# Performance work log

Measured on AMD Instinct MI355X. Metric: run time of the kernel, lower is better.

## Reference

```python
import jax, jax.numpy as jnp
import numpy as np

B, L = 2, 1024
V, D_MODEL, NL = 32, 256, 6
DI, DS, DC, DTR = 512, 16, 4, 16  # d_inner=expand*d_model, d_state, d_conv, dt_rank=d_model/16
NC, MAXL = 10, 2048
ALPHA = 0.1  # observer_alpha


def setup_inputs() -> dict:
    key = jax.random.key(0)
    ks = jax.random.split(key, 16)
    std = 0.02
    emb = std * jax.random.normal(ks[0], (V, D_MODEL), jnp.float32)
    emb = emb.at[0].set(0.0)  # padding_idx=0
    pos_emb = std * jax.random.normal(ks[1], (MAXL, D_MODEL), jnp.float32)
    ln_w = jnp.ones((NL, D_MODEL), jnp.float32)
    ln_b = jnp.zeros((NL, D_MODEL), jnp.float32)
    in_proj_w = std * jax.random.normal(ks[2], (NL, 2 * DI, D_MODEL), jnp.float32)
    conv_w = 0.1 * jax.random.normal(ks[3], (NL, DI, DC), jnp.float32)
    conv_b = jnp.zeros((NL, DI), jnp.float32)
    x_proj_w = std * jax.random.normal(ks[4], (NL, DTR + 2 * DS, DI), jnp.float32)
    dt_proj_w = std * jax.random.normal(ks[5], (NL, DI, DTR), jnp.float32)
    dt_proj_b = jnp.full((NL, DI), -4.6, jnp.float32)  # softplus(-4.6) ~ 0.01 init dt
    A_log = jnp.broadcast_to(jnp.log(jnp.arange(1, DS + 1, dtype=jnp.float32)), (NL, DI, DS)).copy()  # S4D-real
    Dp = jnp.ones((NL, DI), jnp.float32)
    out_proj_w = std * jax.random.normal(ks[6], (NL, D_MODEL, DI), jnp.float32)
    norm_w = jnp.ones((D_MODEL,), jnp.float32)
    norm_b = jnp.zeros((D_MODEL,), jnp.float32)
    cls_w = std * jax.random.normal(ks[7], (NC, D_MODEL), jnp.float32)
    cls_b = jnp.zeros((NC,), jnp.float32)
    x = jax.random.randint(ks[8], (B, L), 0, V, jnp.int64 if jax.config.jax_enable_x64 else jnp.int32)
    mask = jnp.ones((B, L), jnp.int32)
    return dict(emb=emb, pos_emb=pos_emb, ln_w=ln_w, ln_b=ln_b, in_proj_w=in_proj_w,
                conv_w=conv_w, conv_b=conv_b, x_proj_w=x_proj_w, dt_proj_w=dt_proj_w,
                dt_proj_b=dt_proj_b, A_log=A_log, Dp=Dp, out_proj_w=out_proj_w,
                norm_w=norm_w, norm_b=norm_b, cls_w=cls_w, cls_b=cls_b, x=x, mask=mask)


def _ln(x, w, b):
    m = x.mean(-1, keepdims=True)
    v = ((x - m) ** 2).mean(-1, keepdims=True)
    return (x - m) / jnp.sqrt(v + 1e-5) * w + b


def _forward(emb, pos_emb, ln_w, ln_b, in_proj_w, conv_w, conv_b, x_proj_w,
             dt_proj_w, dt_proj_b, A_log, Dp, out_proj_w, norm_w, norm_b,
             cls_w, cls_b, x, mask):
    Bsz, Lsz = x.shape
    h = emb[x] + pos_emb[:Lsz][None, :, :]  # [B,L,D]
    for i in range(NL):
        res = h
        hn = _ln(h, ln_w[i], ln_b[i])
        xz = hn @ in_proj_w[i].T                      # [B,L,2*DI]
        x_in, z = jnp.split(xz, 2, axis=-1)
        # causal depthwise conv1d, kernel DC
        xpad = jnp.pad(x_in, ((0, 0), (DC - 1, 0), (0, 0)))
        xc = conv_b[i]
        for k in range(DC):
            xc = xc + conv_w[i][:, k] * xpad[:, k:k + Lsz, :]
        xc = jax.nn.silu(xc)
        x_dbl = xc @ x_proj_w[i].T                    # [B,L,DTR+2*DS]
        dt = x_dbl[..., :DTR]
        Bm = x_dbl[..., DTR:DTR + DS]
        Cm = x_dbl[..., DTR + DS:]
        delta = jax.nn.softplus(dt @ dt_proj_w[i].T + dt_proj_b[i])  # [B,L,DI]
        A = -jnp.exp(A_log[i])                        # [DI,DS]
        dA = jnp.exp(delta[..., None] * A)            # [B,L,DI,DS]
        dBu = delta[..., None] * Bm[:, :, None, :] * xc[..., None]

        def step(carry, inp):
            hs, hh = carry
            dA_t, dBu_t, c_t = inp
            hs = dA_t * hs + dBu_t                    # true state
            pred = dA_t * hh + dBu_t                  # observer prediction
            hh = pred + ALPHA * (hs - pred)           # Luenberger correction
            y = jnp.einsum('bdn,bn->bd', hh, c_t)
            return (hs, hh), y

        init = (jnp.zeros((Bsz, DI, DS), xc.dtype), jnp.zeros((Bsz, DI, DS), xc.dtype))
        _, ys = jax.lax.scan(step, init,
                             (jnp.moveaxis(dA, 1, 0), jnp.moveaxis(dBu, 1, 0), jnp.moveaxis(Cm, 1, 0)))
        y = jnp.moveaxis(ys, 0, 1) + Dp[i] * xc       # [B,L,DI]
        y = y * jax.nn.silu(z)
        h = y @ out_proj_w[i].T + res
    mf = mask[..., None].astype(h.dtype)
    pooled = (h * mf).sum(axis=1) / mf.sum(axis=1)    # masked mean pool
    pooled = _ln(pooled, norm_w, norm_b)
    return pooled @ cls_w.T + cls_b                   # [B,NC]


def reference(emb, pos_emb, ln_w, ln_b, in_proj_w, conv_w, conv_b, x_proj_w,
              dt_proj_w, dt_proj_b, A_log, Dp, out_proj_w, norm_w, norm_b,
              cls_w, cls_b, x, mask):
    return _forward(emb, pos_emb, ln_w, ln_b, in_proj_w, conv_w, conv_b, x_proj_w,
                    dt_proj_w, dt_proj_b, A_log, Dp, out_proj_w, norm_w, norm_b,
                    cls_w, cls_b, x, mask)
```

## Files before the change

### kernel.cpp

```cpp
#include <hip/hip_runtime.h>
#include <math.h>

#define B_ 2
#define L_ 1024
#define DM 256
#define NL_ 6
#define DI_ 512
#define DS_ 16
#define DC_ 4
#define NC_ 10
#define ALPHA_ 0.1f
#define LC 32
#define NCH (L_/LC)
#define NCHAIN (B_*DI_*DS_)
#define BETA_LC 0.034336838202925124f

typedef unsigned short ushort_t;
typedef __attribute__((ext_vector_type(8))) short s16x8;
typedef __attribute__((ext_vector_type(4))) float f32x4;
typedef __attribute__((ext_vector_type(8))) unsigned short u16x8;

__device__ __forceinline__ float sigmoidf_(float x){ return 1.f/(1.f+__expf(-x)); }
__device__ __forceinline__ ushort_t f2bf(float f){
  union{float f;unsigned u;} c; c.f=f; unsigned u=c.u;
  return (ushort_t)((u + 0x7fffu + ((u>>16)&1u))>>16);
}
__device__ __forceinline__ float bf2f(ushort_t h){
  union{unsigned u;float f;} c; c.u = ((unsigned)h)<<16; return c.f;
}
__device__ __forceinline__ int kidx(int d){ return d + ((d>>7)<<2); }

__global__ void k_embed(const float* __restrict__ emb, const float* __restrict__ pos,
                        const int* __restrict__ ids, float* __restrict__ h){
  int row = blockIdx.x;
  int t = row & (L_-1);
  int d = threadIdx.x;
  int v = ids[row];
  h[(size_t)row*DM + d] = emb[(size_t)v*DM + d] + pos[(size_t)t*DM + d];
}

__global__ void k_cvt2(const float* __restrict__ a, int na, const float* __restrict__ b2,
                       ushort_t* __restrict__ oa, ushort_t* __restrict__ ob, int ntot){
  int i = (blockIdx.x*256 + threadIdx.x)*4;
  if (i >= ntot) return;
  const float* src; ushort_t* dst; int k;
  if (i < na){ src = a; dst = oa; k = i; }
  else       { src = b2; dst = ob; k = i - na; }
  float4 v = *reinterpret_cast<const float4*>(&src[k]);
  ushort4 r;
  r.x = f2bf(v.x); r.y = f2bf(v.y); r.z = f2bf(v.z); r.w = f2bf(v.w);
  *reinterpret_cast<ushort4*>(&dst[k]) = r;
}

__global__ __launch_bounds__(256) void k_gemm_ln(const float* __restrict__ h,
    const ushort_t* __restrict__ W, const float* __restrict__ lw,
    const float* __restrict__ lb, ushort_t* __restrict__ xzb){
  __shared__ ushort_t As[64][264];
  __shared__ ushort_t Ws[64][264];
  int bm = blockIdx.y<<6, bn = blockIdx.x<<6;
  int tid = threadIdx.x;
  {
    int r = tid>>2, q = tid&3;
    const float* src = &h[(size_t)(bm+r)*DM + q*64];
    float4 v[16]; float s1=0.f, s2=0.f;
    #pragma unroll
    for (int i=0;i<16;i++){
      v[i] = *reinterpret_cast<const float4*>(src + i*4);
      s1 += v[i].x+v[i].y+v[i].z+v[i].w;
      s2 += v[i].x*v[i].x+v[i].y*v[i].y+v[i].z*v[i].z+v[i].w*v[i].w;
    }
    s1 += __shfl_xor(s1,1); s2 += __shfl_xor(s2,1);
    s1 += __shfl_xor(s1,2); s2 += __shfl_xor(s2,2);
    float mean = s1*(1.f/DM);
    float rstd = rsqrtf(s2*(1.f/DM) - mean*mean + 1e-5f);
    #pragma unroll
    for (int i=0;i<16;i++){
      int c = q*64 + i*4;
      ushort4 o;
      o.x = f2bf((v[i].x-mean)*rstd*lw[c+0]+lb[c+0]);
      o.y = f2bf((v[i].y-mean)*rstd*lw[c+1]+lb[c+1]);
      o.z = f2bf((v[i].z-mean)*rstd*lw[c+2]+lb[c+2]);
      o.w = f2bf((v[i].w-mean)*rstd*lw[c+3]+lb[c+3]);
      *reinterpret_cast<ushort4*>(&As[r][c]) = o;
    }
    const ushort_t* ws = &W[(size_t)(bn+r)*DM + q*64];
    #pragma unroll
    for (int i=0;i<8;i++)
      *reinterpret_cast<u16x8*>(&Ws[r][q*64+i*8]) = *reinterpret_cast<const u16x8*>(ws + i*8);
  }
  __syncthreads();
  int lane = tid&63, wid = tid>>6;
  int wm = (wid>>1)<<5, wn = (wid&1)<<5;
  int fr = lane&15, fk = (lane>>4)<<3;
  f32x4 acc[2][2] = {};
  #pragma unroll
  for (int k0=0;k0<DM;k0+=32){
    s16x8 a0 = *reinterpret_cast<const s16x8*>(&As[wm+fr][k0+fk]);
    s16x8 a1 = *reinterpret_cast<const s16x8*>(&As[wm+16+fr][k0+fk]);
    s16x8 b0 = *reinterpret_cast<const s16x8*>(&Ws[wn+fr][k0+fk]);
    s16x8 b1 = *reinterpret_cast<const s16x8*>(&Ws[wn+16+fr][k0+fk]);
    acc[0][0] = __builtin_amdgcn_mfma_f32_16x16x32_bf16(a0,b0,acc[0][0],0,0,0);
    acc[0][1] = __builtin_amdgcn_mfma_f32_16x16x32_bf16(a0,b1,acc[0][1],0,0,0);
    acc[1][0] = __builtin_amdgcn_mfma_f32_16x16x32_bf16(a1,b0,acc[1][0],0,0,0);
    acc[1][1] = __builtin_amdgcn_mfma_f32_16x16x32_bf16(a1,b1,acc[1][1],0,0,0);
  }
  int cr = (lane>>4)<<2, cc = lane&15;
  #pragma unroll
  for (int i=0;i<2;i++)
    #pragma unroll
    for (int j=0;j<2;j++){
      int row = bm + wm + (i<<4) + cr;
      int col = bn + wn + (j<<4) + cc;
      #pragma unroll
      for (int r=0;r<4;r++)
        xzb[(size_t)(row+r)*(2*DI_) + col] = f2bf(acc[i][j][r]);
    }
}

__global__ __launch_bounds__(256) void k_xpc(const ushort_t* __restrict__ xzb,
    const float* __restrict__ cw, const float* __restrict__ cb,
    const float* __restrict__ xw, const float* __restrict__ dtw,
    const float* __restrict__ dtb, ushort_t* __restrict__ xcb,
    float* __restrict__ xdbl, ushort_t* __restrict__ deltab){
  __shared__ float sxz[7][DI_];
  __shared__ float sx[4][DI_+16];
  __shared__ float sdbl[4][48];
  int tid = threadIdx.x;
  int m0 = blockIdx.x*4;
  #pragma unroll
  for (int idx=0; idx<14; ++idx){
    int flat = idx*256 + tid;
    int i = flat>>9, d = flat&511;
    int mr = m0 - 3 + i;
    sxz[i][d] = (mr>=0) ? bf2f(xzb[(size_t)mr*(2*DI_) + d]) : 0.f;
  }
  __syncthreads();
  #pragma unroll
  for (int idx=0; idx<8; ++idx){
    int flat = idx*256 + tid;
    int r = flat>>9, d = flat&511;
    int t = (m0 + r) & (L_-1);
    float acc = cb[d];
    #pragma unroll
    for (int k=0;k<4;k++)
      if (t-3+k >= 0) acc = fmaf(cw[d*4+k], sxz[r+k][d], acc);
    float sv = acc * sigmoidf_(acc);
    sx[r][kidx(d)] = sv;
    xcb[(size_t)(m0+r)*DI_ + d] = f2bf(sv);
  }
  __syncthreads();
  if (tid < 192){
    int o = tid>>2, q = tid&3;
    const float* wp = &xw[(size_t)o*DI_ + q*128];
    const int qb = q*132;
    float a0=0.f,a1=0.f,a2=0.f,a3=0.f;
    #pragma unroll 8
    for (int k4=0;k4<32;k4++){
      float4 wv = *reinterpret_cast<const float4*>(wp + k4*4);
      int kk = qb + k4*4;
      float4 x0 = *reinterpret_cast<const float4*>(&sx[0][kk]);
      float4 x1 = *reinterpret_cast<const float4*>(&sx[1][kk]);
      float4 x2 = *reinterpret_cast<const float4*>(&sx[2][kk]);
      float4 x3 = *reinterpret_cast<const float4*>(&sx[3][kk]);
      a0 = fmaf(x0.x,wv.x,a0); a0 = fmaf(x0.y,wv.y,a0); a0 = fmaf(x0.z,wv.z,a0); a0 = fmaf(x0.w,wv.w,a0);
      a1 = fmaf(x1.x,wv.x,a1); a1 = fmaf(x1.y,wv.y,a1); a1 = fmaf(x1.z,wv.z,a1); a1 = fmaf(x1.w,wv.w,a1);
      a2 = fmaf(x2.x,wv.x,a2); a2 = fmaf(x2.y,wv.y,a2); a2 = fmaf(x2.z,wv.z,a2); a2 = fmaf(x2.w,wv.w,a2);
      a3 = fmaf(x3.x,wv.x,a3); a3 = fmaf(x3.y,wv.y,a3); a3 = fmaf(x3.z,wv.z,a3); a3 = fmaf(x3.w,wv.w,a3);
    }
    a0 += __shfl_xor(a0,1); a0 += __shfl_xor(a0,2);
    a1 += __shfl_xor(a1,1); a1 += __shfl_xor(a1,2);
    a2 += __shfl_xor(a2,1); a2 += __shfl_xor(a2,2);
    a3 += __shfl_xor(a3,1); a3 += __shfl_xor(a3,2);
    if (q==0){
      sdbl[0][o]=a0; sdbl[1][o]=a1; sdbl[2][o]=a2; sdbl[3][o]=a3;
      xdbl[(size_t)(m0+0)*48+o]=a0;
      xdbl[(size_t)(m0+1)*48+o]=a1;
      xdbl[(size_t)(m0+2)*48+o]=a2;
      xdbl[(size_t)(m0+3)*48+o]=a3;
    }
  }
  __syncthreads();
  #pragma unroll
  for (int idx=0; idx<8; ++idx){
    int flat = idx*256 + tid;
    int r = flat>>9, n = flat&511;
    const float4* wp = reinterpret_cast<const float4*>(&dtw[n*16]);
    float4 w0=wp[0], w1=wp[1], w2=wp[2], w3=wp[3];
    const float* sd = sdbl[r];
    float acc = dtb[n];
    acc = fmaf(sd[0],w0.x,acc);  acc = fmaf(sd[1],w0.y,acc);
    acc = fmaf(sd[2],w0.z,acc);  acc = fmaf(sd[3],w0.w,acc);
    acc = fmaf(sd[4],w1.x,acc);  acc = fmaf(sd[5],w1.y,acc);
    acc = fmaf(sd[6],w1.z,acc);  acc = fmaf(sd[7],w1.w,acc);
    acc = fmaf(sd[8],w2.x,acc);  acc = fmaf(sd[9],w2.y,acc);
    acc = fmaf(sd[10],w2.z,acc); acc = fmaf(sd[11],w2.w,acc);
    acc = fmaf(sd[12],w3.x,acc); acc = fmaf(sd[13],w3.y,acc);
    acc = fmaf(sd[14],w3.z,acc); acc = fmaf(sd[15],w3.w,acc);
    float sp2 = (acc>20.f)? acc : log1pf(__expf(acc));
    deltab[(size_t)(m0+r)*DI_ + n] = f2bf(sp2);
  }
}

__global__ __launch_bounds__(256) void k_scanA(const ushort_t* __restrict__ deltab,
    const ushort_t* __restrict__ xcb, const float* __restrict__ xdbl,
    const float* __restrict__ A_log, float4* __restrict__ smry){
  int j = blockIdx.x, g = blockIdx.y, b = blockIdx.z;
  int tid = threadIdx.x;
  int n = tid&15, dg = tid>>4;
  int d0 = g*16;
  __shared__ float sdel[LC][16], sxv[LC][16], sB[LC][16];
  if (tid < 128){
    int arr = tid>>6, slot = tid&63, row = slot>>1, half = slot&1;
    int m = b*L_ + j*LC + row;
    const ushort_t* src = arr ? xcb : deltab;
    u16x8 v = *reinterpret_cast<const u16x8*>(&src[(size_t)m*DI_ + d0 + half*8]);
    float* dst = arr ? &sxv[row][half*8] : &sdel[row][half*8];
    #pragma unroll
    for (int i=0;i<8;i++) dst[i] = bf2f((ushort_t)v[i]);
  } else {
    int slot = tid-128;
    int row = slot>>2, c4 = (slot&3)<<2;
    int m = b*L_ + j*LC + row;
    *reinterpret_cast<float4*>(&sB[row][c4]) =
      *reinterpret_cast<const float4*>(&xdbl[(size_t)m*48 + 16 + c4]);
  }
  __syncthreads();
  float a = -__expf(A_log[(d0+dg)*DS_ + n]);
  float hs=0.f, hh=0.f, cp=1.f;
  #pragma unroll
  for (int tt=0; tt<LC; tt+=8){
    float dA8[8], dBu8[8];
    #pragma unroll
    for (int t=0;t<8;t++){
      float dv = sdel[tt+t][dg];
      dA8[t]  = __expf(dv*a);
      dBu8[t] = dv * sxv[tt+t][dg] * sB[tt+t][n];
    }
    #pragma unroll
    for (int t=0;t<8;t++){
      float mix = fmaf(ALPHA_, hs-hh, hh);
      hs = fmaf(dA8[t], hs, dBu8[t]);
      hh = fmaf(dA8[t], mix, dBu8[t]);
      cp *= dA8[t];
    }
  }
  smry[(size_t)j*NCHAIN + (size_t)(b*DI_+d0)*DS_ + tid] = float4{cp,hs,hh,0.f};
}

__global__ __launch_bounds__(256) void k_scanC(const ushort_t* __restrict__ deltab,
    const ushort_t* __restrict__ xcb, const float* __restrict__ xdbl,
    const ushort_t* __restrict__ xzb, const float* __restrict__ A_log,
    const float* __restrict__ Dp, const float4* __restrict__ smry,
    ushort_t* __restrict__ y2b){
  int j = blockIdx.x, g = blockIdx.y, b = blockIdx.z;
  int tid = threadIdx.x;
  int n = tid&15, dg = tid>>4;
  int d0 = g*16;
  __shared__ float sdel[LC][16], sxv[LC][16], sB[LC][16], sC[LC][16], sz[LC][16], sy[LC][16];
  if (tid < 128){
    int arr = tid>>6, slot = tid&63, row = slot>>1, half = slot&1;
    int m = b*L_ + j*LC + row;
    const ushort_t* src = arr ? xcb : deltab;
    u16x8 v = *reinterpret_cast<const u16x8*>(&src[(size_t)m*DI_ + d0 + half*8]);
    float* dst = arr ? &sxv[row][half*8] : &sdel[row][half*8];
    #pragma unroll
    for (int i=0;i<8;i++) dst[i] = bf2f((ushort_t)v[i]);
  } else if (tid < 192){
    int slot = tid-128, row = slot>>1, half = slot&1;
    int m = b*L_ + j*LC + row;
    u16x8 v = *reinterpret_cast<const u16x8*>(&xzb[(size_t)m*(2*DI_) + DI_ + d0 + half*8]);
    #pragma unroll
    for (int i=0;i<8;i++) sz[row][half*8+i] = bf2f((ushort_t)v[i]);
  } else {
    int slot = tid-192;
    #pragma unroll
    for (int k=0;k<4;k++){
      int t4 = slot + k*64;
      int arr = t4>>7, idx4 = t4&127;
      int row = idx4>>2, c4 = (idx4&3)<<2;
      int m = b*L_ + j*LC + row;
      float* dst = arr ? &sC[row][c4] : &sB[row][c4];
      *reinterpret_cast<float4*>(dst) =
        *reinterpret_cast<const float4*>(&xdbl[(size_t)m*48 + 16 + arr*16 + c4]);
    }
  }
  int chain = (b*DI_+d0)*DS_ + tid;
  float hs=0.f, hh=0.f;
  #pragma unroll 4
  for (int jj=0; jj<j; ++jj){
    float4 v = smry[(size_t)jj*NCHAIN + chain];
    float snew = fmaf(v.x, hs, v.y);
    hh = fmaf(v.x, fmaf(BETA_LC, hh-hs, hs), v.z);
    hs = snew;
  }
  __syncthreads();
  float a = -__expf(A_log[(d0+dg)*DS_ + n]);
  #pragma unroll
  for (int tt=0; tt<LC; tt+=8){
    float dA8[8], dBu8[8], yv8[8];
    #pragma unroll
    for (int t=0;t<8;t++){
      float dv = sdel[tt+t][dg];
      dA8[t]  = __expf(dv*a);
      dBu8[t] = dv * sxv[tt+t][dg] * sB[tt+t][n];
    }
    #pragma unroll
    for (int t=0;t<8;t++){
      float mix = fmaf(ALPHA_, hs-hh, hh);
      hs = fmaf(dA8[t], hs, dBu8[t]);
      hh = fmaf(dA8[t], mix, dBu8[t]);
      yv8[t] = hh * sC[tt+t][n];
    }
    #pragma unroll
    for (int t=0;t<8;t++){
      yv8[t] += __shfl_xor(yv8[t],1,16);
      yv8[t] += __shfl_xor(yv8[t],2,16);
      yv8[t] += __shfl_xor(yv8[t],4,16);
      yv8[t] += __shfl_xor(yv8[t],8,16);
    }
    if (n==0){
      #pragma unroll
      for (int t=0;t<8;t++) sy[tt+t][dg] = yv8[t];
    }
  }
  __syncthreads();
  float dpv = Dp[d0 + (tid&15)];
  #pragma unroll
  for (int idx=0; idx<2; ++idx){
    int flat = idx*256 + tid;
    int t2 = flat>>4, dd = flat&15;
    float xvv = sxv[t2][dd];
    float zv  = sz [t2][dd];
    float yfin = (sy[t2][dd] + dpv*xvv) * (zv*sigmoidf_(zv));
    y2b[(size_t)(b*L_ + j*LC + t2)*DI_ + d0 + dd] = f2bf(yfin);
  }
}

__global__ __launch_bounds__(256) void k_gemm_out(const ushort_t* __restrict__ A,
    const ushort_t* __restrict__ W, float* __restrict__ h){
  __shared__ ushort_t As[32][264];
  __shared__ ushort_t Ws[64][264];
  int bm = blockIdx.y<<5, bn = blockIdx.x<<6;
  int tid = threadIdx.x;
  int lane = tid&63, wid = tid>>6;
  int wm = (wid>>1)<<4, wn = (wid&1)<<5;
  int fr = lane&15, fk = (lane>>4)<<3;
  f32x4 acc[2] = {};
  for (int k0=0;k0<DI_;k0+=256){
    {
      int r = tid>>3, q = tid&7;
      const ushort_t* src = &A[(size_t)(bm+r)*DI_ + k0 + q*32];
      #pragma unroll
      for (int i=0;i<4;i++)
        *reinterpret_cast<u16x8*>(&As[r][q*32+i*8]) = *reinterpret_cast<const u16x8*>(src+i*8);
      int r2 = tid>>2, q2 = tid&3;
      const ushort_t* ws = &W[(size_t)(bn+r2)*DI_ + k0 + q2*64];
      #pragma unroll
      for (int i=0;i<8;i++)
        *reinterpret_cast<u16x8*>(&Ws[r2][q2*64+i*8]) = *reinterpret_cast<const u16x8*>(ws+i*8);
    }
    __syncthreads();
    #pragma unroll
    for (int k=0;k<256;k+=32){
      s16x8 a0 = *reinterpret_cast<const s16x8*>(&As[wm+fr][k+fk]);
      s16x8 b0 = *reinterpret_cast<const s16x8*>(&Ws[wn+fr][k+fk]);
      s16x8 b1 = *reinterpret_cast<const s16x8*>(&Ws[wn+16+fr][k+fk]);
      acc[0] = __builtin_amdgcn_mfma_f32_16x16x32_bf16(a0,b0,acc[0],0,0,0);
      acc[1] = __builtin_amdgcn_mfma_f32_16x16x32_bf16(a0,b1,acc[1],0,0,0);
    }
    __syncthreads();
  }
  int cr = (lane>>4)<<2, cc = lane&15;
  #pragma unroll
  for (int jj=0;jj<2;jj++){
    int row = bm + wm + cr;
    int col = bn + wn + (jj<<4) + cc;
    #pragma unroll
    for (int r=0;r<4;r++){
      size_t idx2 = (size_t)(row+r)*DM + col;
      h[idx2] += acc[jj][r];
    }
  }
}

__global__ __launch_bounds__(256) void k_pool(const float* __restrict__ h,
    const int* __restrict__ mask, float* __restrict__ partial){
  int p = blockIdx.x, b = blockIdx.y, d = threadIdx.x;
  int t0 = p*64;
  __shared__ float sm[64];
  if (d < 64) sm[d] = (float)mask[b*L_ + t0 + d];
  __syncthreads();
  const float* hp = &h[(size_t)(b*L_ + t0)*DM + d];
  float s = 0.f;
  #pragma unroll 8
  for (int i=0;i<64;i++)
    s = fmaf(sm[i], hp[(size_t)i*DM], s);
  partial[(size_t)(b*16+p)*DM + d] = s;
}

__global__ __launch_bounds__(256) void k_head(const float* __restrict__ partial,
    const int* __restrict__ mask, const float* __restrict__ nw, const float* __restrict__ nb,
    const float* __restrict__ cw, const float* __restrict__ cb, float* __restrict__ out){
  int b = blockIdx.x, d = threadIdx.x;
  int4 mi = *reinterpret_cast<const int4*>(&mask[b*L_ + d*4]);
  float cnt = (float)(mi.x + mi.y + mi.z + mi.w);
  #pragma unroll
  for (int o=32;o>0;o>>=1) cnt += __shfl_down(cnt,o);
  __shared__ float ac[4];
  __shared__ float scnt;
  int wid = d>>6, lane = d&63;
  if (lane==0) ac[wid] = cnt;
  __syncthreads();
  if (d==0) scnt = ac[0]+ac[1]+ac[2]+ac[3];
  __syncthreads();
  float s = 0.f;
  #pragma unroll
  for (int p=0;p<16;p++) s += partial[(size_t)(b*16+p)*DM + d];
  float v = s / scnt;
  float s1 = v, s2 = v*v;
  #pragma unroll
  for (int o=32;o>0;o>>=1){ s1 += __shfl_down(s1,o); s2 += __shfl_down(s2,o); }
  __shared__ float a1[4], a2[4];
  __shared__ float mv[2];
  if (lane==0){ a1[wid]=s1; a2[wid]=s2; }
  __syncthreads();
  if (d==0){
    float t1=a1[0]+a1[1]+a1[2]+a1[3];
    float t2=a2[0]+a2[1]+a2[2]+a2[3];
    float m = t1/(float)DM;
    mv[0]=m; mv[1]=rsqrtf(t2/(float)DM - m*m + 1e-5f);
  }
  __syncthreads();
  __shared__ float sp[DM];
  sp[d] = (v-mv[0])*mv[1]*nw[d]+nb[d];
  __syncthreads();
  __shared__ float cpart[NC_][16];
  if (d < NC_*16){
    int c = d>>4, q = d&15;
    float acc = 0.f;
    #pragma unroll
    for (int k=0;k<16;k++) acc = fmaf(sp[q*16+k], cw[(size_t)c*DM+q*16+k], acc);
    cpart[c][q] = acc;
  }
  __syncthreads();
  if (d < NC_){
    float acc = cb[d];
    #pragma unroll
    for (int q=0;q<16;q++) acc += cpart[d][q];
    out[b*NC_+d] = acc;
  }
}

extern "C" void kernel_launch(void* const* d_in, const int* in_sizes, int n_in,
                              void* d_out, int out_size, void* d_ws, size_t ws_size,
                              hipStream_t stream){
  const float* emb   = (const float*)d_in[0];
  const float* pos   = (const float*)d_in[1];
  const float* ln_w  = (const float*)d_in[2];
  const float* ln_b  = (const float*)d_in[3];
  const float* ipw   = (const float*)d_in[4];
  const float* cw    = (const float*)d_in[5];
  const float* cb    = (const float*)d_in[6];
  const float* xpw   = (const float*)d_in[7];
  const float* dtw   = (const float*)d_in[8];
  const float* dtb   = (const float*)d_in[9];
  const float* A_log = (const float*)d_in[10];
  const float* Dp    = (const float*)d_in[11];
  const float* opw   = (const float*)d_in[12];
  const float* nw    = (const float*)d_in[13];
  const float* nb    = (const float*)d_in[14];
  const float* clw   = (const float*)d_in[15];
  const float* clb   = (const float*)d_in[16];
  const int*   ids   = (const int*)d_in[17];
  const int*   mask  = (const int*)d_in[18];
  float* out = (float*)d_out;

  float* ws    = (float*)d_ws;
  float* h     = ws;
  float* xdbl  = h + 524288;
  float* part  = xdbl + 98304;
  float4* smry = (float4*)(part + 8192);
  ushort_t* xzb    = (ushort_t*)((float*)smry + 2097152);
  ushort_t* xcb    = xzb + 2097152;
  ushort_t* deltab = xcb + 1048576;
  ushort_t* y2b    = deltab + 1048576;
  ushort_t* ipwb   = y2b + 1048576;
  ushort_t* opwb   = ipwb + 1572864;

  const int NA = 6*2*DI_*DM, NB = 6*DM*DI_;
  k_cvt2<<<dim3((NA+NB)/1024), 256, 0, stream>>>(ipw, NA, opw, ipwb, opwb, NA+NB);
  k_embed<<<dim3(B_*L_), dim3(DM), 0, stream>>>(emb, pos, ids, h);

  for (int l=0; l<NL_; ++l){
    k_gemm_ln<<<dim3(16, 32), 256, 0, stream>>>(
        h, ipwb + (size_t)l*2*DI_*DM, ln_w + l*DM, ln_b + l*DM, xzb);
    k_xpc<<<dim3((B_*L_)/4), 256, 0, stream>>>(
        xzb, cw + l*DI_*DC_, cb + l*DI_, xpw + (size_t)l*48*DI_,
        dtw + (size_t)l*DI_*16, dtb + l*DI_, xcb, xdbl, deltab);
    k_scanA<<<dim3(NCH, DI_/16, B_), 256, 0, stream>>>(
        deltab, xcb, xdbl, A_log + (size_t)l*DI_*DS_, smry);
    k_scanC<<<dim3(NCH, DI_/16, B_), 256, 0, stream>>>(
        deltab, xcb, xdbl, xzb, A_log + (size_t)l*DI_*DS_, Dp + l*DI_,
        smry, y2b);
    k_gemm_out<<<dim3(DM/64, (B_*L_)/32), 256, 0, stream>>>(
        y2b, opwb + (size_t)l*DM*DI_, h);
  }
  k_pool<<<dim3(16, B_), 256, 0, stream>>>(h, mask, part);
  k_head<<<dim3(B_), 256, 0, stream>>>(part, mask, nw, nb, clw, clb, out);
}
```

Before: 477.3 us.

## Fuse whole network into one persistent cooperative kernel with grid syncs

Replaces the ~33 separate kernel launches with a single cooperative persistent kernel that walks every stage (weight conversion, embed, LN+in_proj GEMM, conv/x_proj, chunked scan passes, out_proj, pool, head), separated by grid.sync. The chunk-boundary prefix of the scan becomes its own grid-wide pass that writes initial states. Delta is recomputed inside the scan stages instead of being stored. The out_proj GEMM is split along K and accumulates into h with atomics. This aims to remove launch overhead and inter-kernel gaps, at the cost of grid-barrier latency and atomic contention, plus possibly lower occupancy; the old multi-kernel path remains as a fallback.

```diff
diff --git a/kernel.cpp b/kernel.cpp
--- a/kernel.cpp
+++ b/kernel.cpp
@@ -1,5 +1,8 @@
 #include <hip/hip_runtime.h>
+#include <hip/hip_cooperative_groups.h>
 #include <math.h>
+
+namespace cg = cooperative_groups;
 
 #define B_ 2
 #define L_ 1024
@@ -7,12 +10,11 @@
 #define NL_ 6
 #define DI_ 512
 #define DS_ 16
-#define DC_ 4
 #define NC_ 10
 #define ALPHA_ 0.1f
 #define LC 32
-#define NCH (L_/LC)
-#define NCHAIN (B_*DI_*DS_)
+#define NCH 32
+#define NCHAIN 16384
 #define BETA_LC 0.034336838202925124f
 
 typedef unsigned short ushort_t;
@@ -29,6 +31,453 @@
   union{unsigned u;float f;} c; c.u = ((unsigned)h)<<16; return c.f;
 }
 __device__ __forceinline__ int kidx(int d){ return d + ((d>>7)<<2); }
+
+__global__ __launch_bounds__(256, 2) void k_net(
+    const float* __restrict__ emb, const float* __restrict__ pos,
+    const int* __restrict__ ids, const int* __restrict__ maskp,
+    const float* __restrict__ ln_w, const float* __restrict__ ln_b,
+    const float* __restrict__ ipw, const float* __restrict__ opw,
+    const float* __restrict__ cw_a, const float* __restrict__ cb_a,
+    const float* __restrict__ xw_a, const float* __restrict__ dtw_a,
+    const float* __restrict__ dtb_a, const float* __restrict__ al_a,
+    const float* __restrict__ dp_a,
+    const float* __restrict__ nw, const float* __restrict__ nb,
+    const float* __restrict__ clw, const float* __restrict__ clb,
+    float* __restrict__ outp,
+    float* __restrict__ hbuf, float* __restrict__ xdbl, float* __restrict__ part,
+    float4* __restrict__ smry, float2* __restrict__ initA,
+    ushort_t* __restrict__ xzb, ushort_t* __restrict__ xcb,
+    ushort_t* __restrict__ y2b, ushort_t* __restrict__ ipwb,
+    ushort_t* __restrict__ opwb)
+{
+  cg::grid_group grid = cg::this_grid();
+  __shared__ __align__(16) char smem[26368];
+  const int bid = blockIdx.x, tid = threadIdx.x;
+  const int GS = gridDim.x;
+  const int lane = tid & 63, wv = tid >> 6;
+  const int fr = lane & 15, fk = (lane>>4)<<3;
+  const int cr = (lane>>4)<<2, cc = lane & 15;
+  const int wm16 = (wv>>1)<<4, wn32 = (wv&1)<<5;
+
+  {
+    const int NA = NL_*2*DI_*DM, NBn = NL_*DM*DI_;
+    const int NT4 = (NA+NBn)>>2;
+    for (int i4 = bid*256 + tid; i4 < NT4; i4 += GS*256){
+      int i = i4<<2;
+      const float* s; ushort_t* dst; int k = i;
+      if (i < NA){ s = ipw; dst = ipwb; } else { s = opw; dst = opwb; k = i-NA; }
+      float4 v = *reinterpret_cast<const float4*>(&s[k]);
+      ushort4 r; r.x=f2bf(v.x); r.y=f2bf(v.y); r.z=f2bf(v.z); r.w=f2bf(v.w);
+      *reinterpret_cast<ushort4*>(&dst[k]) = r;
+    }
+    for (int row = bid; row < B_*L_; row += GS)
+      hbuf[(size_t)row*DM + tid] =
+        emb[(size_t)ids[row]*DM + tid] + pos[(size_t)(row & (L_-1))*DM + tid];
+  }
+  grid.sync();
+
+  for (int l=0; l<NL_; ++l){
+    const ushort_t* Wip = ipwb + (size_t)l*2*DI_*DM;
+    const ushort_t* Wop = opwb + (size_t)l*DM*DI_;
+    const float* lw = ln_w + l*DM;  const float* lb = ln_b + l*DM;
+    const float* cw = cw_a + l*DI_*4; const float* cb = cb_a + l*DI_;
+    const float* xw = xw_a + (size_t)l*48*DI_;
+    const float* dtw = dtw_a + (size_t)l*DI_*16;
+    const float* dtb = dtb_a + l*DI_;
+    const float* alog = al_a + (size_t)l*DI_*DS_;
+    const float* Dp = dp_a + l*DI_;
+
+    for (int tile = bid; tile < 1024; tile += GS){
+      int bmt = tile >> 4, bnt = tile & 15;
+      float* smean = (float*)smem;
+      float* srstd = smean + 32;
+      ushort_t* As = (ushort_t*)(smem + 256);
+      ushort_t* Ws = As + 32*72;
+      {
+        int r = tid>>3, s = tid&7;
+        const float* src = &hbuf[(size_t)(bmt*32+r)*DM + s*32];
+        float s1=0.f, s2=0.f;
+        #pragma unroll
+        for (int i=0;i<8;i++){
+          float4 v = *reinterpret_cast<const float4*>(src + i*4);
+          s1 += v.x+v.y+v.z+v.w;
+          s2 += v.x*v.x+v.y*v.y+v.z*v.z+v.w*v.w;
+        }
+        s1 += __shfl_xor(s1,1); s2 += __shfl_xor(s2,1);
+        s1 += __shfl_xor(s1,2); s2 += __shfl_xor(s2,2);
+        s1 += __shfl_xor(s1,4); s2 += __shfl_xor(s2,4);
+        if (s==0){
+          float mean = s1*(1.f/DM);
+          smean[r] = mean;
+          srstd[r] = rsqrtf(s2*(1.f/DM) - mean*mean + 1e-5f);
+        }
+      }
+      __syncthreads();
+      f32x4 acc0 = {}, acc1 = {};
+      for (int kk=0; kk<4; ++kk){
+        {
+          int r = tid>>3, c8 = (tid&7)<<3;
+          float mean = smean[r], rs = srstd[r];
+          const float* src = &hbuf[(size_t)(bmt*32+r)*DM + kk*64 + c8];
+          float4 v0 = *reinterpret_cast<const float4*>(src);
+          float4 v1 = *reinterpret_cast<const float4*>(src+4);
+          const float* lwp = &lw[kk*64+c8];
+          const float* lbp = &lb[kk*64+c8];
+          u16x8 ov;
+          ov[0]=(short)f2bf((v0.x-mean)*rs*lwp[0]+lbp[0]);
+          ov[1]=(short)f2bf((v0.y-mean)*rs*lwp[1]+lbp[1]);
+          ov[2]=(short)f2bf((v0.z-mean)*rs*lwp[2]+lbp[2]);
+          ov[3]=(short)f2bf((v0.w-mean)*rs*lwp[3]+lbp[3]);
+          ov[4]=(short)f2bf((v1.x-mean)*rs*lwp[4]+lbp[4]);
+          ov[5]=(short)f2bf((v1.y-mean)*rs*lwp[5]+lbp[5]);
+          ov[6]=(short)f2bf((v1.z-mean)*rs*lwp[6]+lbp[6]);
+          ov[7]=(short)f2bf((v1.w-mean)*rs*lwp[7]+lbp[7]);
+          *reinterpret_cast<u16x8*>(&As[r*72 + c8]) = ov;
+          int r2 = tid>>2, c16 = (tid&3)<<4;
+          const ushort_t* wsrc = &Wip[(size_t)(bnt*64+r2)*DM + kk*64 + c16];
+          *reinterpret_cast<u16x8*>(&Ws[r2*72+c16])   = *reinterpret_cast<const u16x8*>(wsrc);
+          *reinterpret_cast<u16x8*>(&Ws[r2*72+c16+8]) = *reinterpret_cast<const u16x8*>(wsrc+8);
+        }
+        __syncthreads();
+        #pragma unroll
+        for (int ks=0; ks<64; ks+=32){
+          s16x8 a0 = *reinterpret_cast<const s16x8*>(&As[(wm16+fr)*72 + ks+fk]);
+          s16x8 b0 = *reinterpret_cast<const s16x8*>(&Ws[(wn32+fr)*72 + ks+fk]);
+          s16x8 b1 = *reinterpret_cast<const s16x8*>(&Ws[(wn32+16+fr)*72 + ks+fk]);
+          acc0 = __builtin_amdgcn_mfma_f32_16x16x32_bf16(a0,b0,acc0,0,0,0);
+          acc1 = __builtin_amdgcn_mfma_f32_16x16x32_bf16(a0,b1,acc1,0,0,0);
+        }
+        __syncthreads();
+      }
+      #pragma unroll
+      for (int r=0;r<4;r++){
+        int row = bmt*32 + wm16 + cr + r;
+        xzb[(size_t)row*(2*DI_) + bnt*64 + wn32 + cc]      = f2bf(acc0[r]);
+        xzb[(size_t)row*(2*DI_) + bnt*64 + wn32 + 16 + cc] = f2bf(acc1[r]);
+      }
+    }
+    grid.sync();
+
+    for (int vb = bid; vb < 1024; vb += GS){
+      float* sxz = (float*)smem;
+      float* sx  = sxz + 2560;
+      int m0 = vb*2;
+      for (int t4 = tid; t4 < 320; t4 += 256){
+        int i = t4 >> 6, c8 = (t4 & 63) << 3;
+        int mr = m0 - 3 + i;
+        if (mr >= 0){
+          u16x8 v = *reinterpret_cast<const u16x8*>(&xzb[(size_t)mr*(2*DI_) + c8]);
+          #pragma unroll
+          for (int e=0;e<8;e++) sxz[i*512 + c8 + e] = bf2f((ushort_t)v[e]);
+        } else {
+          #pragma unroll
+          for (int e=0;e<8;e++) sxz[i*512 + c8 + e] = 0.f;
+        }
+      }
+      __syncthreads();
+      {
+        int r = tid >> 7, d4 = (tid & 127) << 2;
+        int m = m0 + r, t = m & (L_-1);
+        ushort4 ov;
+        #pragma unroll
+        for (int e=0;e<4;e++){
+          int d = d4+e;
+          float acc = cb[d];
+          #pragma unroll
+          for (int k=0;k<4;k++)
+            if (t-3+k >= 0) acc = fmaf(cw[d*4+k], sxz[(r+k)*512 + d], acc);
+          float sv = acc * sigmoidf_(acc);
+          sx[r*528 + kidx(d)] = sv;
+          ((ushort_t*)&ov)[e] = f2bf(sv);
+        }
+        *reinterpret_cast<ushort4*>(&xcb[(size_t)m*DI_ + d4]) = ov;
+      }
+      __syncthreads();
+      if (tid < 192){
+        int o = tid>>2, q = tid&3;
+        const float* wp = &xw[(size_t)o*DI_ + q*128];
+        const int qb = q*132;
+        float a0=0.f, a1=0.f;
+        #pragma unroll 8
+        for (int k4=0;k4<32;k4++){
+          float4 wvv = *reinterpret_cast<const float4*>(wp + k4*4);
+          int kk2 = qb + k4*4;
+          float4 x0 = *reinterpret_cast<const float4*>(&sx[kk2]);
+          float4 x1 = *reinterpret_cast<const float4*>(&sx[528 + kk2]);
+          a0 = fmaf(x0.x,wvv.x,a0); a0 = fmaf(x0.y,wvv.y,a0);
+          a0 = fmaf(x0.z,wvv.z,a0); a0 = fmaf(x0.w,wvv.w,a0);
+          a1 = fmaf(x1.x,wvv.x,a1); a1 = fmaf(x1.y,wvv.y,a1);
+          a1 = fmaf(x1.z,wvv.z,a1); a1 = fmaf(x1.w,wvv.w,a1);
+        }
+        a0 += __shfl_xor(a0,1); a0 += __shfl_xor(a0,2);
+        a1 += __shfl_xor(a1,1); a1 += __shfl_xor(a1,2);
+        if (q==0){
+          xdbl[(size_t)m0*48 + o]     = a0;
+          xdbl[(size_t)(m0+1)*48 + o] = a1;
+        }
+      }
+      __syncthreads();
+    }
+    grid.sync();
+
+    for (int vb = bid; vb < 2048; vb += GS){
+      int j = vb >> 6, gb = vb & 63, g = gb >> 1, bb = gb & 1;
+      int d0 = g*16, mbase = bb*L_ + j*LC;
+      float* sbd  = (float*)smem;
+      float* sdtw = sbd + 1536;
+      float* sxv  = sdtw + 256;
+      float* sdel = sxv + 512;
+      {
+        const float4* xsrc = reinterpret_cast<const float4*>(xdbl + (size_t)mbase*48);
+        reinterpret_cast<float4*>(sbd)[tid] = xsrc[tid];
+        if (tid < 128) reinterpret_cast<float4*>(sbd)[256+tid] = xsrc[256+tid];
+        if (tid < 64){
+          int row = tid>>1, half = tid&1;
+          u16x8 v = *reinterpret_cast<const u16x8*>(&xcb[(size_t)(mbase+row)*DI_ + d0 + half*8]);
+          #pragma unroll
+          for (int e=0;e<8;e++) sxv[row*16 + half*8 + e] = bf2f((ushort_t)v[e]);
+        } else if (tid < 128){
+          int s = tid-64, row = s>>2, c4 = (s&3)<<2;
+          *reinterpret_cast<float4*>(&sdtw[row*16+c4]) =
+            *reinterpret_cast<const float4*>(&dtw[(size_t)(d0+row)*16 + c4]);
+        }
+      }
+      __syncthreads();
+      #pragma unroll
+      for (int q=0;q<2;q++){
+        int p = q*256 + tid, t = p>>4, dd = p&15;
+        float acc = dtb[d0+dd];
+        #pragma unroll
+        for (int k=0;k<16;k++) acc = fmaf(sbd[t*48+k], sdtw[dd*16+k], acc);
+        sdel[t*16+dd] = (acc>20.f)? acc : log1pf(__expf(acc));
+      }
+      __syncthreads();
+      int n = tid&15, dg = tid>>4;
+      float a = -__expf(alog[(d0+dg)*DS_ + n]);
+      float hs=0.f, hh=0.f, cp=1.f;
+      #pragma unroll
+      for (int tt=0; tt<LC; tt+=8){
+        float dA8[8], dBu8[8];
+        #pragma unroll
+        for (int t=0;t<8;t++){
+          float dv = sdel[(tt+t)*16 + dg];
+          dA8[t]  = __expf(dv*a);
+          dBu8[t] = dv * sxv[(tt+t)*16 + dg] * sbd[(tt+t)*48 + 16+n];
+        }
+        #pragma unroll
+        for (int t=0;t<8;t++){
+          float mix = fmaf(ALPHA_, hs-hh, hh);
+          hs = fmaf(dA8[t], hs, dBu8[t]);
+          hh = fmaf(dA8[t], mix, dBu8[t]);
+          cp *= dA8[t];
+        }
+      }
+      smry[(size_t)j*NCHAIN + (size_t)(bb*DI_+d0)*DS_ + tid] = float4{cp,hs,hh,0.f};
+      __syncthreads();
+    }
+    grid.sync();
+
+    for (int c = bid*256 + tid; c < NCHAIN; c += GS*256){
+      float hs=0.f, hh=0.f;
+      #pragma unroll
+      for (int j=0;j<NCH;j++){
+        size_t o = (size_t)j*NCHAIN + c;
+        float4 v = smry[o];
+        initA[o] = float2{hs,hh};
+        float snew = fmaf(v.x, hs, v.y);
+        hh = fmaf(v.x, fmaf(BETA_LC, hh-hs, hs), v.z);
+        hs = snew;
+      }
+    }
+    grid.sync();
+
+    for (int vb = bid; vb < 2048; vb += GS){
+      int j = vb >> 6, gb = vb & 63, g = gb >> 1, bb = gb & 1;
+      int d0 = g*16, mbase = bb*L_ + j*LC;
+      float2 iv = initA[(size_t)j*NCHAIN + (size_t)(bb*DI_+d0)*DS_ + tid];
+      float* sbd  = (float*)smem;
+      float* sdtw = sbd + 1536;
+      float* sxv  = sdtw + 256;
+      float* sdel = sxv + 512;
+      float* szv  = sdel + 512;
+      float* sy   = szv + 512;
+      {
+        const float4* xsrc = reinterpret_cast<const float4*>(xdbl + (size_t)mbase*48);
+        reinterpret_cast<float4*>(sbd)[tid] = xsrc[tid];
+        if (tid < 128) reinterpret_cast<float4*>(sbd)[256+tid] = xsrc[256+tid];
+        if (tid < 64){
+          int row = tid>>1, half = tid&1;
+          u16x8 v = *reinterpret_cast<const u16x8*>(&xcb[(size_t)(mbase+row)*DI_ + d0 + half*8]);
+          #pragma unroll
+          for (int e=0;e<8;e++) sxv[row*16 + half*8 + e] = bf2f((ushort_t)v[e]);
+        } else if (tid < 128){
+          int s = tid-64, row = s>>1, half = s&1;
+          u16x8 v = *reinterpret_cast<const u16x8*>(&xzb[(size_t)(mbase+row)*(2*DI_) + DI_ + d0 + half*8]);
+          #pragma unroll
+          for (int e=0;e<8;e++) szv[row*16 + half*8 + e] = bf2f((ushort_t)v[e]);
+        } else if (tid < 192){
+          int s = tid-128, row = s>>2, c4 = (s&3)<<2;
+          *reinterpret_cast<float4*>(&sdtw[row*16+c4]) =
+            *reinterpret_cast<const float4*>(&dtw[(size_t)(d0+row)*16 + c4]);
+        }
+      }
+      __syncthreads();
+      #pragma unroll
+      for (int q=0;q<2;q++){
+        int p = q*256 + tid, t = p>>4, dd = p&15;
+        float acc = dtb[d0+dd];
+        #pragma unroll
+        for (int k=0;k<16;k++) acc = fmaf(sbd[t*48+k], sdtw[dd*16+k], acc);
+        sdel[t*16+dd] = (acc>20.f)? acc : log1pf(__expf(acc));
+      }
+      __syncthreads();
+      int n = tid&15, dg = tid>>4;
+      float a = -__expf(alog[(d0+dg)*DS_ + n]);
+      float hs = iv.x, hh = iv.y;
+      #pragma unroll
+      for (int tt=0; tt<LC; tt+=8){
+        float dA8[8], dBu8[8], yv8[8];
+        #pragma unroll
+        for (int t=0;t<8;t++){
+          float dv = sdel[(tt+t)*16 + dg];
+          dA8[t]  = __expf(dv*a);
+          dBu8[t] = dv * sxv[(tt+t)*16 + dg] * sbd[(tt+t)*48 + 16+n];
+        }
+        #pragma unroll
+        for (int t=0;t<8;t++){
+          float mix = fmaf(ALPHA_, hs-hh, hh);
+          hs = fmaf(dA8[t], hs, dBu8[t]);
+          hh = fmaf(dA8[t], mix, dBu8[t]);
+          yv8[t] = hh * sbd[(tt+t)*48 + 32+n];
+        }
+        #pragma unroll
+        for (int t=0;t<8;t++){
+          yv8[t] += __shfl_xor(yv8[t],1,16);
+          yv8[t] += __shfl_xor(yv8[t],2,16);
+          yv8[t] += __shfl_xor(yv8[t],4,16);
+          yv8[t] += __shfl_xor(yv8[t],8,16);
+        }
+        if (n==0){
+          #pragma unroll
+          for (int t=0;t<8;t++) sy[(tt+t)*16 + dg] = yv8[t];
+        }
+      }
+      __syncthreads();
+      float dpv = Dp[d0 + (tid&15)];
+      #pragma unroll
+      for (int idx=0; idx<2; ++idx){
+        int flat = idx*256 + tid;
+        int t2 = flat>>4, dd = flat&15;
+        float xvv = sxv[t2*16+dd];
+        float zv  = szv[t2*16+dd];
+        float yfin = (sy[t2*16+dd] + dpv*xvv) * (zv*sigmoidf_(zv));
+        y2b[(size_t)(mbase + t2)*DI_ + d0 + dd] = f2bf(yfin);
+      }
+      __syncthreads();
+    }
+    grid.sync();
+
+    for (int vb = bid; vb < 1024; vb += GS){
+      int t5 = vb >> 2, kq = vb & 3;
+      int bmt = t5 >> 2, bnt = t5 & 3;
+      ushort_t* As = (ushort_t*)smem;
+      ushort_t* Ws = As + 32*136;
+      {
+        int r = tid>>3, c16 = (tid&7)<<4;
+        const ushort_t* src = &y2b[(size_t)(bmt*32+r)*DI_ + kq*128 + c16];
+        *reinterpret_cast<u16x8*>(&As[r*136 + c16])   = *reinterpret_cast<const u16x8*>(src);
+        *reinterpret_cast<u16x8*>(&As[r*136 + c16+8]) = *reinterpret_cast<const u16x8*>(src+8);
+        int r2 = tid>>2, c32 = (tid&3)<<5;
+        const ushort_t* wsrc = &Wop[(size_t)(bnt*64+r2)*DI_ + kq*128 + c32];
+        #pragma unroll
+        for (int i=0;i<4;i++)
+          *reinterpret_cast<u16x8*>(&Ws[r2*136 + c32 + i*8]) =
+            *reinterpret_cast<const u16x8*>(wsrc + i*8);
+      }
+      __syncthreads();
+      f32x4 acc0={}, acc1={};
+      #pragma unroll
+      for (int ks=0; ks<128; ks+=32){
+        s16x8 a0 = *reinterpret_cast<const s16x8*>(&As[(wm16+fr)*136 + ks+fk]);
+        s16x8 b0 = *reinterpret_cast<const s16x8*>(&Ws[(wn32+fr)*136 + ks+fk]);
+        s16x8 b1 = *reinterpret_cast<const s16x8*>(&Ws[(wn32+16+fr)*136 + ks+fk]);
+        acc0 = __builtin_amdgcn_mfma_f32_16x16x32_bf16(a0,b0,acc0,0,0,0);
+        acc1 = __builtin_amdgcn_mfma_f32_16x16x32_bf16(a0,b1,acc1,0,0,0);
+      }
+      #pragma unroll
+      for (int r=0;r<4;r++){
+        int row = bmt*32 + wm16 + cr + r;
+        atomicAdd(&hbuf[(size_t)row*DM + bnt*64 + wn32 + cc], acc0[r]);
+        atomicAdd(&hbuf[(size_t)row*DM + bnt*64 + wn32 + 16 + cc], acc1[r]);
+      }
+      __syncthreads();
+    }
+    grid.sync();
+  }
+
+  for (int pb = bid; pb < 32; pb += GS){
+    int p = pb >> 1, bb = pb & 1;
+    float* sm = (float*)smem;
+    if (tid < 64) sm[tid] = (float)maskp[bb*L_ + p*64 + tid];
+    __syncthreads();
+    const float* hp = &hbuf[(size_t)(bb*L_ + p*64)*DM + tid];
+    float s = 0.f;
+    #pragma unroll 8
+    for (int i=0;i<64;i++) s = fmaf(sm[i], hp[(size_t)i*DM], s);
+    part[(size_t)(bb*16+p)*DM + tid] = s;
+    __syncthreads();
+  }
+  grid.sync();
+
+  for (int hb = bid; hb < 2; hb += GS){
+    int b = hb, d = tid;
+    float* sp    = (float*)smem;
+    float* cpart = sp + 256;
+    float* aux   = cpart + 160;
+    int4 mi = *reinterpret_cast<const int4*>(&maskp[b*L_ + d*4]);
+    float cnt = (float)(mi.x + mi.y + mi.z + mi.w);
+    #pragma unroll
+    for (int o=32;o>0;o>>=1) cnt += __shfl_down(cnt,o);
+    int wd = d>>6, ln2 = d&63;
+    if (ln2==0) aux[wd] = cnt;
+    __syncthreads();
+    if (d==0) aux[14] = aux[0]+aux[1]+aux[2]+aux[3];
+    __syncthreads();
+    float s = 0.f;
+    #pragma unroll
+    for (int p=0;p<16;p++) s += part[(size_t)(b*16+p)*DM + d];
+    float v = s / aux[14];
+    float s1 = v, s2 = v*v;
+    #pragma unroll
+    for (int o=32;o>0;o>>=1){ s1 += __shfl_down(s1,o); s2 += __shfl_down(s2,o); }
+    if (ln2==0){ aux[4+wd]=s1; aux[8+wd]=s2; }
+    __syncthreads();
+    if (d==0){
+      float t1=aux[4]+aux[5]+aux[6]+aux[7];
+      float t2=aux[8]+aux[9]+aux[10]+aux[11];
+      float m = t1/(float)DM;
+      aux[12]=m; aux[13]=rsqrtf(t2/(float)DM - m*m + 1e-5f);
+    }
+    __syncthreads();
+    sp[d] = (v-aux[12])*aux[13]*nw[d]+nb[d];
+    __syncthreads();
+    if (d < NC_*16){
+      int c = d>>4, q = d&15;
+      float acc = 0.f;
+      #pragma unroll
+      for (int k=0;k<16;k++) acc = fmaf(sp[q*16+k], clw[(size_t)c*DM+q*16+k], acc);
+      cpart[c*16+q] = acc;
+    }
+    __syncthreads();
+    if (d < NC_){
+      float acc = clb[d];
+      #pragma unroll
+      for (int q=0;q<16;q++) acc += cpart[d*16+q];
+      outp[b*NC_+d] = acc;
+    }
+    __syncthreads();
+  }
+}
 
 __global__ void k_embed(const float* __restrict__ emb, const float* __restrict__ pos,
                         const int* __restrict__ ids, float* __restrict__ h){
@@ -128,25 +577,38 @@
   int tid = threadIdx.x;
   int m0 = blockIdx.x*4;
   #pragma unroll
-  for (int idx=0; idx<14; ++idx){
-    int flat = idx*256 + tid;
-    int i = flat>>9, d = flat&511;
-    int mr = m0 - 3 + i;
-    sxz[i][d] = (mr>=0) ? bf2f(xzb[(size_t)mr*(2*DI_) + d]) : 0.f;
-  }
-  __syncthreads();
-  #pragma unroll
-  for (int idx=0; idx<8; ++idx){
-    int flat = idx*256 + tid;
-    int r = flat>>9, d = flat&511;
+  for (int q=0;q<2;q++){
+    int idx = q*256 + tid;
+    if (idx < 448){
+      int i = idx>>6, c8 = (idx&63)<<3;
+      int mr = m0 - 3 + i;
+      if (mr >= 0){
+        u16x8 v = *reinterpret_cast<const u16x8*>(&xzb[(size_t)mr*(2*DI_) + c8]);
+        #pragma unroll
+        for (int e=0;e<8;e++) sxz[i][c8+e] = bf2f((ushort_t)v[e]);
+      } else {
+        #pragma unroll
+        for (int e=0;e<8;e++) sxz[i][c8+e] = 0.f;
+      }
+    }
+  }
+  __syncthreads();
+  {
+    int r = tid>>6, c8 = (tid&63)<<3;
     int t = (m0 + r) & (L_-1);
-    float acc = cb[d];
-    #pragma unroll
-    for (int k=0;k<4;k++)
-      if (t-3+k >= 0) acc = fmaf(cw[d*4+k], sxz[r+k][d], acc);
-    float sv = acc * sigmoidf_(acc);
-    sx[r][kidx(d)] = sv;
-    xcb[(size_t)(m0+r)*DI_ + d] = f2bf(sv);
+    u16x8 outv;
+    #pragma unroll
+    for (int e=0;e<8;e++){
+      int d = c8 + e;
+      float acc = cb[d];
+      #pragma unroll
+      for (int k=0;k<4;k++)
+        if (t-3+k >= 0) acc = fmaf(cw[d*4+k], sxz[r+k][d], acc);
+      float sv = acc * sigmoidf_(acc);
+      sx[r][kidx(d)] = sv;
+      outv[e] = (short)f2bf(sv);
+    }
+    *reinterpret_cast<u16x8*>(&xcb[(size_t)(m0+r)*DI_ + c8]) = outv;
   }
   __syncthreads();
   if (tid < 192){
@@ -480,31 +942,58 @@
   float* xdbl  = h + 524288;
   float* part  = xdbl + 98304;
   float4* smry = (float4*)(part + 8192);
-  ushort_t* xzb    = (ushort_t*)((float*)smry + 2097152);
+  float2* initA= (float2*)((float*)smry + 2097152);
+  ushort_t* xzb    = (ushort_t*)((float*)initA + 1048576);
   ushort_t* xcb    = xzb + 2097152;
   ushort_t* deltab = xcb + 1048576;
   ushort_t* y2b    = deltab + 1048576;
   ushort_t* ipwb   = y2b + 1048576;
   ushort_t* opwb   = ipwb + 1572864;
 
-  const int NA = 6*2*DI_*DM, NB = 6*DM*DI_;
-  k_cvt2<<<dim3((NA+NB)/1024), 256, 0, stream>>>(ipw, NA, opw, ipwb, opwb, NA+NB);
-  k_embed<<<dim3(B_*L_), dim3(DM), 0, stream>>>(emb, pos, ids, h);
-
-  for (int l=0; l<NL_; ++l){
-    k_gemm_ln<<<dim3(16, 32), 256, 0, stream>>>(
-        h, ipwb + (size_t)l*2*DI_*DM, ln_w + l*DM, ln_b + l*DM, xzb);
-    k_xpc<<<dim3((B_*L_)/4), 256, 0, stream>>>(
-        xzb, cw + l*DI_*DC_, cb + l*DI_, xpw + (size_t)l*48*DI_,
-        dtw + (size_t)l*DI_*16, dtb + l*DI_, xcb, xdbl, deltab);
-    k_scanA<<<dim3(NCH, DI_/16, B_), 256, 0, stream>>>(
-        deltab, xcb, xdbl, A_log + (size_t)l*DI_*DS_, smry);
-    k_scanC<<<dim3(NCH, DI_/16, B_), 256, 0, stream>>>(
-        deltab, xcb, xdbl, xzb, A_log + (size_t)l*DI_*DS_, Dp + l*DI_,
-        smry, y2b);
-    k_gemm_out<<<dim3(DM/64, (B_*L_)/32), 256, 0, stream>>>(
-        y2b, opwb + (size_t)l*DM*DI_, h);
-  }
-  k_pool<<<dim3(16, B_), 256, 0, stream>>>(h, mask, part);
-  k_head<<<dim3(B_), 256, 0, stream>>>(part, mask, nw, nb, clw, clb, out);
-}
+  bool done = false;
+  int dev = 0;
+  (void)hipGetDevice(&dev);
+  int coop = 0;
+  (void)hipDeviceGetAttribute(&coop, hipDeviceAttributeCooperativeLaunch, dev);
+  int occ = 0;
+  (void)hipOccupancyMaxActiveBlocksPerMultiprocessor(&occ, k_net, 256, 0);
+  if (coop && occ > 0){
+    int grid = occ * 256;
+    if (grid > 1024) grid = 1024;
+    void* args[] = {
+      (void*)&emb, (void*)&pos, (void*)&ids, (void*)&mask,
+      (void*)&ln_w, (void*)&ln_b, (void*)&ipw, (void*)&opw,
+      (void*)&cw, (void*)&cb, (void*)&xpw, (void*)&dtw, (void*)&dtb,
+      (void*)&A_log, (void*)&Dp, (void*)&nw, (void*)&nb, (void*)&clw, (void*)&clb,
+      (void*)&out,
+      (void*)&h, (void*)&xdbl, (void*)&part, (void*)&smry, (void*)&initA,
+      (void*)&xzb, (void*)&xcb, (void*)&y2b, (void*)&ipwb, (void*)&opwb
+    };
+    hipError_t err = hipLaunchCooperativeKernel((void*)k_net, dim3(grid), dim3(256),
+                                                args, 0, stream);
+    if (err == hipSuccess) done = true;
+    else (void)hipGetLastError();
+  }
+
+  if (!done){
+    const int NA = 6*2*DI_*DM, NB = 6*DM*DI_;
+    k_cvt2<<<dim3((NA+NB)/1024), 256, 0, stream>>>(ipw, NA, opw, ipwb, opwb, NA+NB);
+    k_embed<<<dim3(B_*L_), dim3(DM), 0, stream>>>(emb, pos, ids, h);
+    for (int l=0; l<NL_; ++l){
+      k_gemm_ln<<<dim3(16, 32), 256, 0, stream>>>(
+          h, ipwb + (size_t)l*2*DI_*DM, ln_w + l*DM, ln_b + l*DM, xzb);
+      k_xpc<<<dim3((B_*L_)/4), 256, 0, stream>>>(
+          xzb, cw + l*DI_*4, cb + l*DI_, xpw + (size_t)l*48*DI_,
+          dtw + (size_t)l*DI_*16, dtb + l*DI_, xcb, xdbl, deltab);
+      k_scanA<<<dim3(NCH, DI_/16, B_), 256, 0, stream>>>(
+          deltab, xcb, xdbl, A_log + (size_t)l*DI_*DS_, smry);
+      k_scanC<<<dim3(NCH, DI_/16, B_), 256, 0, stream>>>(
+          deltab, xcb, xdbl, xzb, A_log + (size_t)l*DI_*DS_, Dp + l*DI_,
+          smry, y2b);
+      k_gemm_out<<<dim3(DM/64, (B_*L_)/32), 256, 0, stream>>>(
+          y2b, opwb + (size_t)l*DM*DI_, h);
+    }
+    k_pool<<<dim3(16, B_), 256, 0, stream>>>(h, mask, part);
+    k_head<<<dim3(B_), 256, 0, stream>>>(part, mask, nw, nb, clw, clb, out);
+  }
+}
```

After: 1.871 ms. 292% more time.
